# Kernel tuning notes

Measured on AMD Instinct MI355X. Metric: run time of the kernel, lower is better.

## Reference

```python
import jax, jax.numpy as jnp
import numpy as np


def _rms_norm(x, eps=1e-5):
    x32 = x.astype(jnp.float32)
    var = jnp.mean(x32 * x32, axis=-1, keepdims=True)
    return (x32 * jax.lax.rsqrt(var + eps)).astype(x.dtype)


def _rotate_half(x):
    x1, x2 = jnp.split(x, 2, axis=-1)
    return jnp.concatenate([-x2, x1], axis=-1)


def setup_inputs() -> dict:
    key = jax.random.key(0)
    ks = jax.random.split(key, 8)
    B, N, d, dh = 1, 4096, 1024, 64
    inner, k = 2816, 3
    # realistic RoPE cache [N, dh]
    pos = jnp.arange(N, dtype=jnp.float32)[:, None]
    inv = 1.0 / (10000.0 ** (jnp.arange(0, dh, 2, dtype=jnp.float32) / dh))
    ang = pos * inv[None, :]
    ang = jnp.concatenate([ang, ang], axis=-1)
    return {
        'Q_in': jax.random.normal(ks[0], (B, N, d), jnp.float32),
        'cos': jnp.cos(ang),
        'sin': jnp.sin(ang),
        'W_qkv': jax.random.normal(ks[1], (d, 3 * d), jnp.float32) * 0.02,
        'W_o': jax.random.normal(ks[2], (d, d), jnp.float32) * 0.02,
        'W_up': jax.random.normal(ks[3], (d, 2 * inner), jnp.float32) * 0.02,
        'conv_w': jax.random.normal(ks[4], (k, 1, inner), jnp.float32) * 0.1,
        'conv_b': jax.random.normal(ks[5], (inner,), jnp.float32) * 0.01,
        'W_down': jax.random.normal(ks[6], (inner, d), jnp.float32) * 0.02,
    }


def reference(Q_in, cos, sin, W_qkv, W_o, W_up, conv_w, conv_b, W_down):
    B, N, d = Q_in.shape
    H = 16
    dh = d // H
    qkv = (Q_in @ W_qkv).reshape(B, N, 3, H, dh)
    Qp, Kp, Vp = qkv[:, :, 0], qkv[:, :, 1], qkv[:, :, 2]
    # RoPE: cos/sin [N, dh] broadcast over batch and heads
    cb = cos[None, :, None, :]
    sb = sin[None, :, None, :]
    Qp = Qp * cb + _rotate_half(Qp) * sb
    Kp = Kp * cb + _rotate_half(Kp) * sb
    Q = _rms_norm(jnp.transpose(Qp, (0, 2, 1, 3)))  # [B,H,N,dh]
    K = _rms_norm(jnp.transpose(Kp, (0, 2, 1, 3)))
    V = jnp.transpose(Vp, (0, 2, 1, 3))
    # (elu+1)^2 positive-kernel attention (full N x N matrix, as in the source)
    S = jnp.einsum('bhnd,bhmd->bhnm', Q, K) * (dh ** -0.5)
    W = jax.nn.elu(S) + 1.0
    W = W * W  # kernel_power == 2
    Attr = jnp.einsum('bhnm,bhmd->bhnd', W, V)
    C = Attr / (jnp.sum(W, axis=-1, keepdims=True) + 1e-6)
    m = C - V
    m_concat = jnp.transpose(m, (0, 2, 1, 3)).reshape(B, N, d)
    Q_interact = _rms_norm(Q_in + m_concat @ W_o)
    # ConvSwiGLU FFN
    GU = Q_interact @ W_up
    G, U = jnp.split(GU, 2, axis=-1)
    Hf = jax.nn.silu(G) * U  # [B,N,inner]
    Hc = jax.lax.conv_general_dilated(
        Hf, conv_w, window_strides=(1,), padding=[(1, 1)],
        dimension_numbers=('NWC', 'WIO', 'NWC'),
        feature_group_count=Hf.shape[-1])
    Hc = jax.nn.silu(Hc + conv_b)
    return _rms_norm(Q_interact + Hc @ W_down)
```

## Files before the change

### kernel.cpp

```cpp
#include <hip/hip_runtime.h>
#include <hip/hip_bf16.h>
#include <cstdint>

#define N_TOK   4096
#define D_MODEL 1024
#define N_HEAD  16
#define DH      64
#define INNER   2816

typedef __attribute__((ext_vector_type(8))) short bf16x8;
typedef __attribute__((ext_vector_type(4))) float f32x4;
typedef __attribute__((ext_vector_type(8))) unsigned short us8v;
typedef __attribute__((ext_vector_type(4))) unsigned short us4v;

union BF16x8U { bf16x8 v; uint32_t u[4]; };

__device__ __forceinline__ unsigned short f2bf(float x) {
    union { __hip_bfloat16 h; unsigned short u; } c;
    c.h = __float2bfloat16(x);
    return c.u;
}

__device__ __forceinline__ float bf2f(unsigned short u) {
    union { float f; uint32_t i; } c;
    c.i = ((uint32_t)u) << 16;
    return c.f;
}

__device__ __forceinline__ float silu_f(float x) {
    return x / (1.f + __expf(-x));
}

__device__ __forceinline__ void gld16(const unsigned short* g, unsigned short* l) {
    __builtin_amdgcn_global_load_lds(
        (const __attribute__((address_space(1))) void*)g,
        (__attribute__((address_space(3))) void*)l, 16, 0, 0);
}

__global__ __launch_bounds__(256) void cvt_bf16(
    const float* __restrict__ in, unsigned short* __restrict__ out) {
    const size_t i8 = ((size_t)blockIdx.x * 256 + threadIdx.x) * 8;
    float4 a = *reinterpret_cast<const float4*>(&in[i8]);
    float4 b = *reinterpret_cast<const float4*>(&in[i8 + 4]);
    us8v o;
    o[0] = f2bf(a.x); o[1] = f2bf(a.y); o[2] = f2bf(a.z); o[3] = f2bf(a.w);
    o[4] = f2bf(b.x); o[5] = f2bf(b.y); o[6] = f2bf(b.z); o[7] = f2bf(b.w);
    *reinterpret_cast<us8v*>(&out[i8]) = o;
}

__global__ __launch_bounds__(256) void transpose_bf16(
    const float* __restrict__ W, unsigned short* __restrict__ WT,
    int K, int N) {
    __shared__ unsigned short T[64][65];
    const int n0 = blockIdx.x * 64;
    const int k0 = blockIdx.y * 64;
    const int t = threadIdx.x;
#pragma unroll
    for (int i = 0; i < 4; ++i) {
        const int id = i * 256 + t;
        const int r = id >> 4;
        const int c = (id & 15) * 4;
        float4 v = *reinterpret_cast<const float4*>(
            &W[(size_t)(k0 + r) * N + n0 + c]);
        T[c + 0][r] = f2bf(v.x);
        T[c + 1][r] = f2bf(v.y);
        T[c + 2][r] = f2bf(v.z);
        T[c + 3][r] = f2bf(v.w);
    }
    __syncthreads();
#pragma unroll
    for (int i = 0; i < 2; ++i) {
        const int id = i * 256 + t;
        const int n = id >> 3;
        const int c = (id & 7) * 8;
        us8v o;
#pragma unroll
        for (int j = 0; j < 8; ++j) o[j] = T[n][c + j];
        *reinterpret_cast<us8v*>(&WT[(size_t)(n0 + n) * K + k0 + c]) = o;
    }
}

template<int OBF>
__global__ __launch_bounds__(256) void gemm_bf16(
    const unsigned short* __restrict__ A, const unsigned short* __restrict__ Bt,
    void* __restrict__ Cout, int M, int N, int K) {
    __shared__ unsigned short As[128 * 64];
    __shared__ unsigned short Bs[128 * 64];
    const int tid = threadIdx.x;
    const int lane = tid & 63;
    const int w = tid >> 6;
    const int l15 = lane & 15, lg = lane >> 4;
    const int wm = w >> 1, wn = w & 1;
    const int rowBase = blockIdx.y * 128;
    const int colBase = blockIdx.x * 128;

    const int srow = w * 32 + (lane >> 3);
    const int scol = (lane & 7) * 8;
    const unsigned short* Ag = &A[(size_t)(rowBase + srow) * K + scol];
    const unsigned short* Bg = &Bt[(size_t)(colBase + srow) * K + scol];

    f32x4 acc[4][4];
#pragma unroll
    for (int i = 0; i < 4; ++i)
#pragma unroll
        for (int j = 0; j < 4; ++j) acc[i][j] = (f32x4){0.f, 0.f, 0.f, 0.f};

    for (int k0 = 0; k0 < K; k0 += 64) {
#pragma unroll
        for (int j = 0; j < 4; ++j) {
            gld16(Ag + (size_t)j * 8 * K + k0, &As[(w * 32 + j * 8) * 64]);
            gld16(Bg + (size_t)j * 8 * K + k0, &Bs[(w * 32 + j * 8) * 64]);
        }
        __syncthreads();
        bf16x8 af[2][4], bfr[2][4];
#pragma unroll
        for (int kk = 0; kk < 2; ++kk) {
#pragma unroll
            for (int f = 0; f < 4; ++f) {
                af[kk][f] = *reinterpret_cast<const bf16x8*>(
                    &As[(wm * 64 + f * 16 + l15) * 64 + kk * 32 + lg * 8]);
                bfr[kk][f] = *reinterpret_cast<const bf16x8*>(
                    &Bs[(wn * 64 + f * 16 + l15) * 64 + kk * 32 + lg * 8]);
            }
        }
#pragma unroll
        for (int kk = 0; kk < 2; ++kk)
#pragma unroll
            for (int mf = 0; mf < 4; ++mf)
#pragma unroll
                for (int nf = 0; nf < 4; ++nf)
                    acc[mf][nf] = __builtin_amdgcn_mfma_f32_16x16x32_bf16(
                        bfr[kk][nf], af[kk][mf], acc[mf][nf], 0, 0, 0);
        __syncthreads();
    }
#pragma unroll
    for (int mf = 0; mf < 4; ++mf) {
#pragma unroll
        for (int nf = 0; nf < 4; ++nf) {
            const size_t m = rowBase + wm * 64 + mf * 16 + l15;
            const size_t n = colBase + wn * 64 + nf * 16 + lg * 4;
            if (OBF) {
                us4v o;
                o[0] = f2bf(acc[mf][nf][0]); o[1] = f2bf(acc[mf][nf][1]);
                o[2] = f2bf(acc[mf][nf][2]); o[3] = f2bf(acc[mf][nf][3]);
                *reinterpret_cast<us4v*>(
                    &((unsigned short*)Cout)[m * N + n]) = o;
            } else {
                float4 o;
                o.x = acc[mf][nf][0]; o.y = acc[mf][nf][1];
                o.z = acc[mf][nf][2]; o.w = acc[mf][nf][3];
                *reinterpret_cast<float4*>(&((float*)Cout)[m * N + n]) = o;
            }
        }
    }
}

template<int OBF>
__global__ __launch_bounds__(256) void gemm_bf16_t64(
    const unsigned short* __restrict__ A, const unsigned short* __restrict__ Bt,
    void* __restrict__ Cout, int M, int N, int K) {
    __shared__ unsigned short As[64 * 64];
    __shared__ unsigned short Bs[128 * 64];
    const int tid = threadIdx.x;
    const int lane = tid & 63;
    const int w = tid >> 6;
    const int l15 = lane & 15, lg = lane >> 4;
    const int rowBase = blockIdx.y * 64;
    const int colBase = blockIdx.x * 128;

    const int srowA = w * 16 + (lane >> 3);
    const int srowB = w * 32 + (lane >> 3);
    const int scol = (lane & 7) * 8;
    const unsigned short* Ag = &A[(size_t)(rowBase + srowA) * K + scol];
    const unsigned short* Bg = &Bt[(size_t)(colBase + srowB) * K + scol];

    f32x4 acc[4][2];
#pragma unroll
    for (int i = 0; i < 4; ++i)
#pragma unroll
        for (int j = 0; j < 2; ++j) acc[i][j] = (f32x4){0.f, 0.f, 0.f, 0.f};

    for (int k0 = 0; k0 < K; k0 += 64) {
#pragma unroll
        for (int j = 0; j < 2; ++j)
            gld16(Ag + (size_t)j * 8 * K + k0, &As[(w * 16 + j * 8) * 64]);
#pragma unroll
        for (int j = 0; j < 4; ++j)
            gld16(Bg + (size_t)j * 8 * K + k0, &Bs[(w * 32 + j * 8) * 64]);
        __syncthreads();
        bf16x8 af[2][4], bfr[2][2];
#pragma unroll
        for (int kk = 0; kk < 2; ++kk) {
#pragma unroll
            for (int f = 0; f < 4; ++f)
                af[kk][f] = *reinterpret_cast<const bf16x8*>(
                    &As[(f * 16 + l15) * 64 + kk * 32 + lg * 8]);
#pragma unroll
            for (int f = 0; f < 2; ++f)
                bfr[kk][f] = *reinterpret_cast<const bf16x8*>(
                    &Bs[(w * 32 + f * 16 + l15) * 64 + kk * 32 + lg * 8]);
        }
#pragma unroll
        for (int kk = 0; kk < 2; ++kk)
#pragma unroll
            for (int mf = 0; mf < 4; ++mf)
#pragma unroll
                for (int nf = 0; nf < 2; ++nf)
                    acc[mf][nf] = __builtin_amdgcn_mfma_f32_16x16x32_bf16(
                        bfr[kk][nf], af[kk][mf], acc[mf][nf], 0, 0, 0);
        __syncthreads();
    }
#pragma unroll
    for (int mf = 0; mf < 4; ++mf) {
#pragma unroll
        for (int nf = 0; nf < 2; ++nf) {
            const size_t m = rowBase + mf * 16 + l15;
            const size_t n = colBase + w * 32 + nf * 16 + lg * 4;
            if (OBF) {
                us4v o;
                o[0] = f2bf(acc[mf][nf][0]); o[1] = f2bf(acc[mf][nf][1]);
                o[2] = f2bf(acc[mf][nf][2]); o[3] = f2bf(acc[mf][nf][3]);
                *reinterpret_cast<us4v*>(
                    &((unsigned short*)Cout)[m * N + n]) = o;
            } else {
                float4 o;
                o.x = acc[mf][nf][0]; o.y = acc[mf][nf][1];
                o.z = acc[mf][nf][2]; o.w = acc[mf][nf][3];
                *reinterpret_cast<float4*>(&((float*)Cout)[m * N + n]) = o;
            }
        }
    }
}

__global__ __launch_bounds__(256) void rope_norm2(
    const float* __restrict__ qkv, const float* __restrict__ cosb,
    const float* __restrict__ sinb, unsigned short* __restrict__ Qb,
    unsigned short* __restrict__ Kb, unsigned short* __restrict__ Vt,
    unsigned short* __restrict__ Vb) {
    const int h = blockIdx.y;
    const int n0 = blockIdx.x * 64;
    const int wv = threadIdx.x >> 6;
    const int lane = threadIdx.x & 63;
    __shared__ unsigned short Vs[64][66];
#pragma unroll 1
    for (int it = 0; it < 16; ++it) {
        const int tn = it * 4 + wv;
        const int n = n0 + tn;
        const float* base = qkv + (size_t)n * (3 * D_MODEL) + h * DH;
        float qv = base[lane];
        float kv = base[D_MODEL + lane];
        float vv = base[2 * D_MODEL + lane];
        const float c = cosb[n * DH + lane];
        const float s = sinb[n * DH + lane];
        const float qp = __shfl(qv, lane ^ 32, 64);
        const float kp = __shfl(kv, lane ^ 32, 64);
        const float sgn = (lane < 32) ? -1.f : 1.f;
        qv = qv * c + sgn * qp * s;
        kv = kv * c + sgn * kp * s;
        float sq = qv * qv, sk = kv * kv;
#pragma unroll
        for (int off = 32; off > 0; off >>= 1) {
            sq += __shfl_xor(sq, off, 64);
            sk += __shfl_xor(sk, off, 64);
        }
        qv *= rsqrtf(sq * (1.f / DH) + 1e-5f) * 0.125f;
        kv *= rsqrtf(sk * (1.f / DH) + 1e-5f);
        const size_t o = ((size_t)h * N_TOK + n) * DH + lane;
        Qb[o] = f2bf(qv);
        Kb[o] = f2bf(kv);
        Vb[o] = f2bf(vv);
        Vs[tn][lane] = f2bf(vv);
    }
    __syncthreads();
    const int d = threadIdx.x >> 2;
    const int c0 = (threadIdx.x & 3) * 16;
    us8v o0, o1;
#pragma unroll
    for (int i = 0; i < 8; ++i) o0[i] = Vs[c0 + i][d];
#pragma unroll
    for (int i = 0; i < 8; ++i) o1[i] = Vs[c0 + 8 + i][d];
    unsigned short* dst = Vt + ((size_t)h * DH + d) * N_TOK + n0 + c0;
    *reinterpret_cast<us8v*>(dst) = o0;
    *reinterpret_cast<us8v*>(dst + 8) = o1;
}

__global__ __launch_bounds__(256, 2) void attn_mfma2(
    const unsigned short* __restrict__ Qb, const unsigned short* __restrict__ Kb,
    const unsigned short* __restrict__ Vt, const unsigned short* __restrict__ Vb,
    unsigned short* __restrict__ Mout) {
    const int B = blockIdx.x;
    const int h = ((B & 7) << 1) | ((B >> 3) & 1);
    const int q0 = (B >> 4) * 64;
    const int lane = threadIdx.x & 63;
    const int wv = threadIdx.x >> 6;
    const int l15 = lane & 15, lg = lane >> 4;
    const unsigned short* Qh = Qb + (size_t)h * N_TOK * DH;
    const unsigned short* Kh = Kb + (size_t)h * N_TOK * DH;
    const unsigned short* Vth = Vt + (size_t)h * DH * N_TOK;

    bf16x8 qf[4][2];
#pragma unroll
    for (int qs = 0; qs < 4; ++qs) {
        const unsigned short* qp = Qh + (size_t)(q0 + qs * 16 + l15) * DH + lg * 8;
        qf[qs][0] = *reinterpret_cast<const bf16x8*>(qp);
        qf[qs][1] = *reinterpret_cast<const bf16x8*>(qp + 32);
    }

    f32x4 ct[4][4];
#pragma unroll
    for (int i = 0; i < 4; ++i)
#pragma unroll
        for (int j = 0; j < 4; ++j) ct[i][j] = (f32x4){0.f, 0.f, 0.f, 0.f};
    float dpart[4] = {0.f, 0.f, 0.f, 0.f};

    const int sA = l15 + ((lg & 1) << 5);
    const int sB = sA + 16;
    const bool hi = (lg & 2) != 0;

#pragma unroll 1
    for (int kt = 0; kt < 16; ++kt) {
        const int k0 = (wv * 16 + kt) * 64;
        const unsigned short* kp = Kh + (size_t)(k0 + l15) * DH + lg * 8;
        bf16x8 kf[4][2];
#pragma unroll
        for (int ks = 0; ks < 4; ++ks) {
            kf[ks][0] = *reinterpret_cast<const bf16x8*>(kp + ks * 16 * DH);
            kf[ks][1] = *reinterpret_cast<const bf16x8*>(kp + ks * 16 * DH + 32);
        }
        const unsigned short* vp = Vth + (size_t)l15 * N_TOK + k0 + lg * 8;
        bf16x8 vf[4][2];
#pragma unroll
        for (int ds = 0; ds < 4; ++ds) {
            vf[ds][0] = *reinterpret_cast<const bf16x8*>(vp + (size_t)ds * 16 * N_TOK);
            vf[ds][1] = *reinterpret_cast<const bf16x8*>(vp + (size_t)ds * 16 * N_TOK + 32);
        }
#pragma unroll
        for (int qs = 0; qs < 4; ++qs) {
            f32x4 st[4];
            __builtin_amdgcn_s_setprio(1);
#pragma unroll
            for (int ks = 0; ks < 4; ++ks) {
                f32x4 z = (f32x4){0.f, 0.f, 0.f, 0.f};
                z = __builtin_amdgcn_mfma_f32_16x16x32_bf16(kf[ks][0], qf[qs][0], z, 0, 0, 0);
                st[ks] = __builtin_amdgcn_mfma_f32_16x16x32_bf16(kf[ks][1], qf[qs][1], z, 0, 0, 0);
            }
            __builtin_amdgcn_s_setprio(0);
            uint32_t wpk[4][2];
#pragma unroll
            for (int ks = 0; ks < 4; ++ks) {
                float w4[4];
#pragma unroll
                for (int r = 0; r < 4; ++r) {
                    const float x = st[ks][r];
                    float e = fmaxf(x, 0.f) + __expf(fminf(x, 0.f));
                    e = e * e;
                    w4[r] = e;
                    dpart[qs] += e;
                }
                wpk[ks][0] = (uint32_t)f2bf(w4[0]) | ((uint32_t)f2bf(w4[1]) << 16);
                wpk[ks][1] = (uint32_t)f2bf(w4[2]) | ((uint32_t)f2bf(w4[3]) << 16);
            }
#pragma unroll
            for (int kh = 0; kh < 2; ++kh) {
                const uint32_t a0 = (uint32_t)__shfl((int)wpk[2 * kh][0], sA, 64);
                const uint32_t a1 = (uint32_t)__shfl((int)wpk[2 * kh][1], sA, 64);
                const uint32_t a2 = (uint32_t)__shfl((int)wpk[2 * kh][0], sB, 64);
                const uint32_t a3 = (uint32_t)__shfl((int)wpk[2 * kh][1], sB, 64);
                const uint32_t b0 = (uint32_t)__shfl((int)wpk[2 * kh + 1][0], sA, 64);
                const uint32_t b1 = (uint32_t)__shfl((int)wpk[2 * kh + 1][1], sA, 64);
                const uint32_t b2 = (uint32_t)__shfl((int)wpk[2 * kh + 1][0], sB, 64);
                const uint32_t b3 = (uint32_t)__shfl((int)wpk[2 * kh + 1][1], sB, 64);
                BF16x8U bb;
                bb.u[0] = hi ? b0 : a0;
                bb.u[1] = hi ? b1 : a1;
                bb.u[2] = hi ? b2 : a2;
                bb.u[3] = hi ? b3 : a3;
                __builtin_amdgcn_s_setprio(1);
#pragma unroll
                for (int ds = 0; ds < 4; ++ds)
                    ct[qs][ds] = __builtin_amdgcn_mfma_f32_16x16x32_bf16(
                        vf[ds][kh], bb.v, ct[qs][ds], 0, 0, 0);
                __builtin_amdgcn_s_setprio(0);
            }
        }
    }

    __shared__ float accs2[2][64][72];
    __shared__ float dens[4][64];
#pragma unroll
    for (int qs = 0; qs < 4; ++qs) {
        float dp = dpart[qs];
        dp += __shfl_xor(dp, 16, 64);
        dp += __shfl_xor(dp, 32, 64);
        if (lg == 0) dens[wv][qs * 16 + l15] = dp;
    }
    if (wv >= 2) {
#pragma unroll
        for (int qs = 0; qs < 4; ++qs)
#pragma unroll
            for (int ds = 0; ds < 4; ++ds)
                *reinterpret_cast<f32x4*>(
                    &accs2[wv - 2][qs * 16 + l15][ds * 16 + lg * 4]) = ct[qs][ds];
    }
    __syncthreads();
    if (wv < 2) {
#pragma unroll
        for (int qs = 0; qs < 4; ++qs)
#pragma unroll
            for (int ds = 0; ds < 4; ++ds)
                ct[qs][ds] += *reinterpret_cast<const f32x4*>(
                    &accs2[wv][qs * 16 + l15][ds * 16 + lg * 4]);
        if (wv == 1) {
#pragma unroll
            for (int qs = 0; qs < 4; ++qs)
#pragma unroll
                for (int ds = 0; ds < 4; ++ds)
                    *reinterpret_cast<f32x4*>(
                        &accs2[1][qs * 16 + l15][ds * 16 + lg * 4]) = ct[qs][ds];
        }
    }
    __syncthreads();
    if (wv == 0) {
#pragma unroll
        for (int qs = 0; qs < 4; ++qs) {
            const int q = qs * 16 + l15;
            const float dnq = 1.f /
                (dens[0][q] + dens[1][q] + dens[2][q] + dens[3][q] + 1e-6f);
            const unsigned short* Vrow = Vb + ((size_t)h * N_TOK + q0 + q) * DH;
            unsigned short* Mrow = Mout + (size_t)(q0 + q) * D_MODEL + h * DH;
#pragma unroll
            for (int ds = 0; ds < 4; ++ds) {
                const int d = ds * 16 + lg * 4;
                const f32x4 s1 = *reinterpret_cast<const f32x4*>(&accs2[1][q][d]);
                const us4v vv = *reinterpret_cast<const us4v*>(&Vrow[d]);
                us4v o;
#pragma unroll
                for (int r = 0; r < 4; ++r)
                    o[r] = f2bf((ct[qs][ds][r] + s1[r]) * dnq - bf2f(vv[r]));
                *reinterpret_cast<us4v*>(&Mrow[d]) = o;
            }
        }
    }
}

template<int WB>
__global__ __launch_bounds__(256) void rms_resid2(
    const float* __restrict__ X, const float* __restrict__ R,
    float* __restrict__ O32, unsigned short* __restrict__ Obf) {
    const int row = blockIdx.x;
    const int tid = threadIdx.x;
    const float4 xv = reinterpret_cast<const float4*>(X + (size_t)row * D_MODEL)[tid];
    const float4 rv = reinterpret_cast<const float4*>(R + (size_t)row * D_MODEL)[tid];
    const float t0 = xv.x + rv.x, t1 = xv.y + rv.y, t2 = xv.z + rv.z, t3 = xv.w + rv.w;
    float ss = t0 * t0 + t1 * t1 + t2 * t2 + t3 * t3;
#pragma unroll
    for (int off = 32; off > 0; off >>= 1) ss += __shfl_xor(ss, off, 64);
    __shared__ float red[4];
    if ((tid & 63) == 0) red[tid >> 6] = ss;
    __syncthreads();
    const float tot = red[0] + red[1] + red[2] + red[3];
    const float rs = rsqrtf(tot * (1.f / D_MODEL) + 1e-5f);
    float4 o;
    o.x = t0 * rs; o.y = t1 * rs; o.z = t2 * rs; o.w = t3 * rs;
    reinterpret_cast<float4*>(O32 + (size_t)row * D_MODEL)[tid] = o;
    if (WB) {
        us4v ob;
        ob[0] = f2bf(o.x); ob[1] = f2bf(o.y); ob[2] = f2bf(o.z); ob[3] = f2bf(o.w);
        *reinterpret_cast<us4v*>(&Obf[(size_t)row * D_MODEL + tid * 4]) = ob;
    }
}

__global__ __launch_bounds__(256) void dwconv_fused(
    const unsigned short* __restrict__ GU, const float* __restrict__ W,
    const float* __restrict__ Bv, unsigned short* __restrict__ Hc) {
    const size_t idx = (size_t)blockIdx.x * 256 + threadIdx.x;
    const int c8 = (int)(idx % (INNER / 8)) * 8;
    const int n = (int)(idx / (INNER / 8));
    float a[8];
    {
        float4 b0 = *reinterpret_cast<const float4*>(&Bv[c8]);
        float4 b1 = *reinterpret_cast<const float4*>(&Bv[c8 + 4]);
        a[0] = b0.x; a[1] = b0.y; a[2] = b0.z; a[3] = b0.w;
        a[4] = b1.x; a[5] = b1.y; a[6] = b1.z; a[7] = b1.w;
    }
#pragma unroll
    for (int k = 0; k < 3; ++k) {
        const int nn = n + k - 1;
        if (nn >= 0 && nn < N_TOK) {
            const unsigned short* row = &GU[(size_t)nn * (2 * INNER)];
            us8v g = *reinterpret_cast<const us8v*>(&row[c8]);
            us8v u = *reinterpret_cast<const us8v*>(&row[INNER + c8]);
            float4 w0 = *reinterpret_cast<const float4*>(&W[(size_t)k * INNER + c8]);
            float4 w1 = *reinterpret_cast<const float4*>(&W[(size_t)k * INNER + c8 + 4]);
            const float wv[8] = {w0.x, w0.y, w0.z, w0.w, w1.x, w1.y, w1.z, w1.w};
#pragma unroll
            for (int j = 0; j < 8; ++j) {
                const float hf = silu_f(bf2f(g[j])) * bf2f(u[j]);
                a[j] += hf * wv[j];
            }
        }
    }
    us8v o;
#pragma unroll
    for (int j = 0; j < 8; ++j) o[j] = f2bf(silu_f(a[j]));
    *reinterpret_cast<us8v*>(&Hc[(size_t)n * INNER + c8]) = o;
}

extern "C" void kernel_launch(void* const* d_in, const int* in_sizes, int n_in,
                              void* d_out, int out_size, void* d_ws, size_t ws_size,
                              hipStream_t stream) {
    const float* Qin   = (const float*)d_in[0];
    const float* cosb  = (const float*)d_in[1];
    const float* sinb  = (const float*)d_in[2];
    const float* Wqkv  = (const float*)d_in[3];
    const float* Wo    = (const float*)d_in[4];
    const float* Wup   = (const float*)d_in[5];
    const float* convw = (const float*)d_in[6];
    const float* convb = (const float*)d_in[7];
    const float* Wdown = (const float*)d_in[8];
    float* out = (float*)d_out;
    float* ws  = (float*)d_ws;

    unsigned short* WqkvT  = (unsigned short*)(ws);
    unsigned short* WoT    = (unsigned short*)(ws + 1572864);
    unsigned short* WupT   = (unsigned short*)(ws + 2097152);
    unsigned short* WdownT = (unsigned short*)(ws + 4980736);
    unsigned short* Qin_bf = (unsigned short*)(ws + 6422528);
    unsigned short* mcat   = (unsigned short*)(ws + 6422528);
    float*          qkv32  = ws + 8519680;
    float*          wo32   = ws + 8519680;
    unsigned short* GU     = (unsigned short*)(ws + 8519680);
    float*          dn32   = ws + 14286848;
    unsigned short* Qb     = (unsigned short*)(ws + 21102592);
    unsigned short* Kb     = (unsigned short*)(ws + 23199744);
    unsigned short* Vt     = (unsigned short*)(ws + 25296896);
    unsigned short* Vb     = (unsigned short*)(ws + 27394048);
    unsigned short* Hc     = (unsigned short*)(ws + 21102592);
    float*          Qi32   = ws + 29491200;
    unsigned short* Qi_bf  = (unsigned short*)(ws + 33685504);

    const dim3 blk(256);
    cvt_bf16<<<2048, blk, 0, stream>>>(Qin, Qin_bf);
    transpose_bf16<<<dim3(48, 16), blk, 0, stream>>>(Wqkv, WqkvT, 1024, 3072);
    transpose_bf16<<<dim3(16, 16), blk, 0, stream>>>(Wo, WoT, 1024, 1024);
    transpose_bf16<<<dim3(88, 16), blk, 0, stream>>>(Wup, WupT, 1024, 5632);
    transpose_bf16<<<dim3(16, 44), blk, 0, stream>>>(Wdown, WdownT, 2816, 1024);
    gemm_bf16<0><<<dim3(24, 32), blk, 0, stream>>>(
        Qin_bf, WqkvT, qkv32, 4096, 3072, 1024);
    rope_norm2<<<dim3(64, 16), blk, 0, stream>>>(qkv32, cosb, sinb, Qb, Kb, Vt, Vb);
    attn_mfma2<<<1024, blk, 0, stream>>>(Qb, Kb, Vt, Vb, mcat);
    gemm_bf16_t64<0><<<dim3(8, 64), blk, 0, stream>>>(
        mcat, WoT, wo32, 4096, 1024, 1024);
    rms_resid2<1><<<4096, blk, 0, stream>>>(wo32, Qin, Qi32, Qi_bf);
    gemm_bf16<1><<<dim3(44, 32), blk, 0, stream>>>(
        Qi_bf, WupT, GU, 4096, 5632, 1024);
    dwconv_fused<<<5632, blk, 0, stream>>>(GU, convw, convb, Hc);
    gemm_bf16_t64<0><<<dim3(8, 64), blk, 0, stream>>>(
        Hc, WdownT, dn32, 4096, 1024, 2816);
    rms_resid2<0><<<4096, blk, 0, stream>>>(dn32, Qi32, out, nullptr);
}
```

Baseline: 439.3 us.

## Emit QKV GEMM in bf16 and split-K the down projection

```diff
diff --git a/kernel.cpp b/kernel.cpp
--- a/kernel.cpp
+++ b/kernel.cpp
@@ -83,7 +83,7 @@
 template<int OBF>
 __global__ __launch_bounds__(256) void gemm_bf16(
     const unsigned short* __restrict__ A, const unsigned short* __restrict__ Bt,
-    void* __restrict__ Cout, int M, int N, int K) {
+    void* __restrict__ Cout, int M, int N, int K, int lda) {
     __shared__ unsigned short As[128 * 64];
     __shared__ unsigned short Bs[128 * 64];
     const int tid = threadIdx.x;
@@ -93,11 +93,12 @@
     const int wm = w >> 1, wn = w & 1;
     const int rowBase = blockIdx.y * 128;
     const int colBase = blockIdx.x * 128;
+    const size_t koff = (size_t)blockIdx.z * K;
 
     const int srow = w * 32 + (lane >> 3);
     const int scol = (lane & 7) * 8;
-    const unsigned short* Ag = &A[(size_t)(rowBase + srow) * K + scol];
-    const unsigned short* Bg = &Bt[(size_t)(colBase + srow) * K + scol];
+    const unsigned short* Ag = &A[(size_t)(rowBase + srow) * lda + koff + scol];
+    const unsigned short* Bg = &Bt[(size_t)(colBase + srow) * lda + koff + scol];
 
     f32x4 acc[4][4];
 #pragma unroll
@@ -108,8 +109,8 @@
     for (int k0 = 0; k0 < K; k0 += 64) {
 #pragma unroll
         for (int j = 0; j < 4; ++j) {
-            gld16(Ag + (size_t)j * 8 * K + k0, &As[(w * 32 + j * 8) * 64]);
-            gld16(Bg + (size_t)j * 8 * K + k0, &Bs[(w * 32 + j * 8) * 64]);
+            gld16(Ag + (size_t)j * 8 * lda + k0, &As[(w * 32 + j * 8) * 64]);
+            gld16(Bg + (size_t)j * 8 * lda + k0, &Bs[(w * 32 + j * 8) * 64]);
         }
         __syncthreads();
         bf16x8 af[2][4], bfr[2][4];
@@ -144,12 +145,13 @@
                 o[0] = f2bf(acc[mf][nf][0]); o[1] = f2bf(acc[mf][nf][1]);
                 o[2] = f2bf(acc[mf][nf][2]); o[3] = f2bf(acc[mf][nf][3]);
                 *reinterpret_cast<us4v*>(
-                    &((unsigned short*)Cout)[m * N + n]) = o;
+                    &((unsigned short*)Cout)[(size_t)blockIdx.z * M * N + m * N + n]) = o;
             } else {
                 float4 o;
                 o.x = acc[mf][nf][0]; o.y = acc[mf][nf][1];
                 o.z = acc[mf][nf][2]; o.w = acc[mf][nf][3];
-                *reinterpret_cast<float4*>(&((float*)Cout)[m * N + n]) = o;
+                *reinterpret_cast<float4*>(
+                    &((float*)Cout)[(size_t)blockIdx.z * M * N + m * N + n]) = o;
             }
         }
     }
@@ -233,7 +235,7 @@
 }
 
 __global__ __launch_bounds__(256) void rope_norm2(
-    const float* __restrict__ qkv, const float* __restrict__ cosb,
+    const unsigned short* __restrict__ qkv, const float* __restrict__ cosb,
     const float* __restrict__ sinb, unsigned short* __restrict__ Qb,
     unsigned short* __restrict__ Kb, unsigned short* __restrict__ Vt,
     unsigned short* __restrict__ Vb) {
@@ -246,10 +248,10 @@
     for (int it = 0; it < 16; ++it) {
         const int tn = it * 4 + wv;
         const int n = n0 + tn;
-        const float* base = qkv + (size_t)n * (3 * D_MODEL) + h * DH;
-        float qv = base[lane];
-        float kv = base[D_MODEL + lane];
-        float vv = base[2 * D_MODEL + lane];
+        const unsigned short* base = qkv + (size_t)n * (3 * D_MODEL) + h * DH;
+        float qv = bf2f(base[lane]);
+        float kv = bf2f(base[D_MODEL + lane]);
+        float vv = bf2f(base[2 * D_MODEL + lane]);
         const float c = cosb[n * DH + lane];
         const float s = sinb[n * DH + lane];
         const float qp = __shfl(qv, lane ^ 32, 64);
@@ -268,8 +270,9 @@
         const size_t o = ((size_t)h * N_TOK + n) * DH + lane;
         Qb[o] = f2bf(qv);
         Kb[o] = f2bf(kv);
-        Vb[o] = f2bf(vv);
-        Vs[tn][lane] = f2bf(vv);
+        Vb[o] = base[2 * D_MODEL + lane];
+        Vs[tn][lane] = base[2 * D_MODEL + lane];
+        (void)vv;
     }
     __syncthreads();
     const int d = threadIdx.x >> 2;
@@ -470,6 +473,29 @@
     }
 }
 
+__global__ __launch_bounds__(256) void rms_resid3(
+    const float* __restrict__ Xa, const float* __restrict__ Xb,
+    const float* __restrict__ R, float* __restrict__ O32) {
+    const int row = blockIdx.x;
+    const int tid = threadIdx.x;
+    const float4 av = reinterpret_cast<const float4*>(Xa + (size_t)row * D_MODEL)[tid];
+    const float4 bv = reinterpret_cast<const float4*>(Xb + (size_t)row * D_MODEL)[tid];
+    const float4 rv = reinterpret_cast<const float4*>(R + (size_t)row * D_MODEL)[tid];
+    const float t0 = av.x + bv.x + rv.x, t1 = av.y + bv.y + rv.y;
+    const float t2 = av.z + bv.z + rv.z, t3 = av.w + bv.w + rv.w;
+    float ss = t0 * t0 + t1 * t1 + t2 * t2 + t3 * t3;
+#pragma unroll
+    for (int off = 32; off > 0; off >>= 1) ss += __shfl_xor(ss, off, 64);
+    __shared__ float red[4];
+    if ((tid & 63) == 0) red[tid >> 6] = ss;
+    __syncthreads();
+    const float tot = red[0] + red[1] + red[2] + red[3];
+    const float rs = rsqrtf(tot * (1.f / D_MODEL) + 1e-5f);
+    float4 o;
+    o.x = t0 * rs; o.y = t1 * rs; o.z = t2 * rs; o.w = t3 * rs;
+    reinterpret_cast<float4*>(O32 + (size_t)row * D_MODEL)[tid] = o;
+}
+
 __global__ __launch_bounds__(256) void dwconv_fused(
     const unsigned short* __restrict__ GU, const float* __restrict__ W,
     const float* __restrict__ Bv, unsigned short* __restrict__ Hc) {
@@ -527,10 +553,10 @@
     unsigned short* WdownT = (unsigned short*)(ws + 4980736);
     unsigned short* Qin_bf = (unsigned short*)(ws + 6422528);
     unsigned short* mcat   = (unsigned short*)(ws + 6422528);
-    float*          qkv32  = ws + 8519680;
+    unsigned short* qkv_bf = (unsigned short*)(ws + 8519680);
     float*          wo32   = ws + 8519680;
     unsigned short* GU     = (unsigned short*)(ws + 8519680);
-    float*          dn32   = ws + 14286848;
+    float*          dn32   = ws + 8519680;
     unsigned short* Qb     = (unsigned short*)(ws + 21102592);
     unsigned short* Kb     = (unsigned short*)(ws + 23199744);
     unsigned short* Vt     = (unsigned short*)(ws + 25296896);
@@ -545,17 +571,17 @@
     transpose_bf16<<<dim3(16, 16), blk, 0, stream>>>(Wo, WoT, 1024, 1024);
     transpose_bf16<<<dim3(88, 16), blk, 0, stream>>>(Wup, WupT, 1024, 5632);
     transpose_bf16<<<dim3(16, 44), blk, 0, stream>>>(Wdown, WdownT, 2816, 1024);
-    gemm_bf16<0><<<dim3(24, 32), blk, 0, stream>>>(
-        Qin_bf, WqkvT, qkv32, 4096, 3072, 1024);
-    rope_norm2<<<dim3(64, 16), blk, 0, stream>>>(qkv32, cosb, sinb, Qb, Kb, Vt, Vb);
+    gemm_bf16<1><<<dim3(24, 32), blk, 0, stream>>>(
+        Qin_bf, WqkvT, qkv_bf, 4096, 3072, 1024, 1024);
+    rope_norm2<<<dim3(64, 16), blk, 0, stream>>>(qkv_bf, cosb, sinb, Qb, Kb, Vt, Vb);
     attn_mfma2<<<1024, blk, 0, stream>>>(Qb, Kb, Vt, Vb, mcat);
     gemm_bf16_t64<0><<<dim3(8, 64), blk, 0, stream>>>(
         mcat, WoT, wo32, 4096, 1024, 1024);
     rms_resid2<1><<<4096, blk, 0, stream>>>(wo32, Qin, Qi32, Qi_bf);
     gemm_bf16<1><<<dim3(44, 32), blk, 0, stream>>>(
-        Qi_bf, WupT, GU, 4096, 5632, 1024);
+        Qi_bf, WupT, GU, 4096, 5632, 1024, 1024);
     dwconv_fused<<<5632, blk, 0, stream>>>(GU, convw, convb, Hc);
-    gemm_bf16_t64<0><<<dim3(8, 64), blk, 0, stream>>>(
-        Hc, WdownT, dn32, 4096, 1024, 2816);
-    rms_resid2<0><<<4096, blk, 0, stream>>>(dn32, Qi32, out, nullptr);
-}
+    gemm_bf16<0><<<dim3(8, 32, 2), blk, 0, stream>>>(
+        Hc, WdownT, dn32, 4096, 1024, 1408, 2816);
+    rms_resid3<<<4096, blk, 0, stream>>>(dn32, dn32 + 4194304, Qi32, out);
+}
```

Result: no change. 432.9 us (-1.5%).
